# Kernel tuning notes

Measured on AMD Instinct MI355X. Metric: run time of the kernel, lower is better.

The kernel has to match this reference:

```python
import jax, jax.numpy as jnp
import numpy as np

Q_ZERO = 8  # Q4_0 zero point: w = scale * (q - 8)


def setup_inputs() -> dict:
    key = jax.random.key(0)
    k_x, k_q, k_s, k_b = jax.random.split(key, 4)
    out_f, in_f, block = 11008, 4096, 32
    n_blocks = in_f // block  # 128
    x = jax.random.normal(k_x, (1, 16, in_f), dtype=jnp.float32)
    # 4-bit quantized values per block (0..15), stored as int32 for jax friendliness
    qweight = jax.random.randint(k_q, (out_f, n_blocks, block), 0, 16, dtype=jnp.int32)
    # per-block fp scales (small, like real ggml scales)
    scales = jax.random.uniform(k_s, (out_f, n_blocks), dtype=jnp.float32) * 0.02
    bias = jax.random.normal(k_b, (out_f,), dtype=jnp.float32) * 0.01
    return {"x": x, "qweight": qweight, "scales": scales, "bias": bias}


def reference(x, qweight, scales, bias):
    # ggml_dequantize (Q4_0): w = scale * (q - 8), per block of 32 along infeatures
    out_f, n_blocks, block = qweight.shape
    w = scales[:, :, None] * (qweight.astype(jnp.float32) - Q_ZERO)  # [out, nb, 32]
    w = w.reshape(out_f, n_blocks * block)  # [out, in]
    # x @ W.T + bias, preserving leading dims
    y = jnp.einsum("bsi,oi->bso", x, w) + bias
    return y
```

## Files before the change

kernel.cpp:

```cpp
#include <hip/hip_runtime.h>
#include <stdint.h>


typedef __attribute__((ext_vector_type(8))) short bf16x8;
typedef __attribute__((ext_vector_type(4))) float f32x4;

#define OUT_F 11008
#define IN_F  4096
#define NB    128
#define KSPLIT 8
#define QB_BLK (NB / KSPLIT)
#define QB_WV  (QB_BLK / 4)
#define NTILES (OUT_F / 16)
#define M_TOK 16

__global__ __launch_bounds__(256, 4)
void qgemm_kernel(const float* __restrict__ x,
                  const int* __restrict__ qw,
                  const float* __restrict__ scales,
                  const float* __restrict__ bias,
                  float* __restrict__ out,
                  float* __restrict__ part) {
  __shared__ uint4 stage[4][QB_WV][128];
  __shared__ float red[4][256];

  const int bid  = blockIdx.x;
  const int kq   = bid & (KSPLIT - 1);
  const int ob   = (bid >> 3) << 4;
  const int tid  = threadIdx.x;
  const int wave = tid >> 6;
  const int lane = tid & 63;
  const int col  = lane & 15;
  const int kr   = lane >> 4;

  const int kb0 = kq * QB_BLK + wave * QB_WV;

  const char* qrow = (const char*)(qw + (size_t)(ob + col) * IN_F)
                   + (size_t)kb0 * 128 + kr * 32;

#pragma unroll
  for (int s = 0; s < QB_WV; ++s) {
    __builtin_amdgcn_global_load_lds(
        (const __attribute__((address_space(1))) void*)(qrow + s * 128),
        (__attribute__((address_space(3))) void*)(&stage[wave][s][0]),
        16, 0, 0);
    __builtin_amdgcn_global_load_lds(
        (const __attribute__((address_space(1))) void*)(qrow + s * 128 + 16),
        (__attribute__((address_space(3))) void*)(&stage[wave][s][64]),
        16, 0, 0);
  }

  const float* xb = x + col * IN_F + kb0 * 32 + kr * 8;
  f32x4 xv[QB_WV][2];
#pragma unroll
  for (int s = 0; s < QB_WV; ++s) {
    xv[s][0] = *(const f32x4*)(xb + s * 32);
    xv[s][1] = *(const f32x4*)(xb + s * 32 + 4);
  }
  f32x4 sv = *(const f32x4*)(scales + (ob + col) * NB + kb0);

  __syncthreads();

  f32x4 acc = {0.f, 0.f, 0.f, 0.f};
#pragma unroll
  for (int s = 0; s < QB_WV; ++s) {
    uint4 q0 = stage[wave][s][lane];
    uint4 q1 = stage[wave][s][64 + lane];
    float sc  = sv[s];
    float m8s = -8.f * sc;
    union { uint32_t u[4]; bf16x8 v; } A, B;
    uint32_t a0 = __float_as_uint(xv[s][0].x) + 0x8000u;
    uint32_t a1 = __float_as_uint(xv[s][0].y) + 0x8000u;
    uint32_t a2 = __float_as_uint(xv[s][0].z) + 0x8000u;
    uint32_t a3 = __float_as_uint(xv[s][0].w) + 0x8000u;
    uint32_t a4 = __float_as_uint(xv[s][1].x) + 0x8000u;
    uint32_t a5 = __float_as_uint(xv[s][1].y) + 0x8000u;
    uint32_t a6 = __float_as_uint(xv[s][1].z) + 0x8000u;
    uint32_t a7 = __float_as_uint(xv[s][1].w) + 0x8000u;
    A.u[0] = __builtin_amdgcn_perm(a1, a0, 0x07060302u);
    A.u[1] = __builtin_amdgcn_perm(a3, a2, 0x07060302u);
    A.u[2] = __builtin_amdgcn_perm(a5, a4, 0x07060302u);
    A.u[3] = __builtin_amdgcn_perm(a7, a6, 0x07060302u);
    uint32_t w0 = __float_as_uint(fmaf((float)(int)q0.x, sc, m8s));
    uint32_t w1 = __float_as_uint(fmaf((float)(int)q0.y, sc, m8s));
    uint32_t w2 = __float_as_uint(fmaf((float)(int)q0.z, sc, m8s));
    uint32_t w3 = __float_as_uint(fmaf((float)(int)q0.w, sc, m8s));
    uint32_t w4 = __float_as_uint(fmaf((float)(int)q1.x, sc, m8s));
    uint32_t w5 = __float_as_uint(fmaf((float)(int)q1.y, sc, m8s));
    uint32_t w6 = __float_as_uint(fmaf((float)(int)q1.z, sc, m8s));
    uint32_t w7 = __float_as_uint(fmaf((float)(int)q1.w, sc, m8s));
    B.u[0] = __builtin_amdgcn_perm(w1, w0, 0x07060302u);
    B.u[1] = __builtin_amdgcn_perm(w3, w2, 0x07060302u);
    B.u[2] = __builtin_amdgcn_perm(w5, w4, 0x07060302u);
    B.u[3] = __builtin_amdgcn_perm(w7, w6, 0x07060302u);
    acc = __builtin_amdgcn_mfma_f32_16x16x32_bf16(A.v, B.v, acc, 0, 0, 0);
  }

#pragma unroll
  for (int r = 0; r < 4; ++r)
    red[wave][(kr * 4 + r) * 16 + col] = acc[r];
  __syncthreads();

  float v = red[0][tid] + red[1][tid] + red[2][tid] + red[3][tid];
  if (part) {
    part[(size_t)bid * 256 + tid] = v;
  } else {
    int t = tid >> 4;
    int o = ob + (tid & 15);
    if (kq == 0) v += bias[o];
    __hip_atomic_fetch_add(out + (size_t)t * OUT_F + o, v, __ATOMIC_RELAXED,
                           __HIP_MEMORY_SCOPE_AGENT);
  }
}

__global__ __launch_bounds__(256)
void reduce_kernel(const float* __restrict__ part,
                   const float* __restrict__ bias,
                   float* __restrict__ out) {
  int idx = blockIdx.x * 256 + threadIdx.x;
  int t = idx / OUT_F;
  int o = idx - t * OUT_F;
  const float* p = part + (size_t)(o >> 4) * (KSPLIT * 256)
                 + ((t << 4) | (o & 15));
  float acc = bias[o];
#pragma unroll
  for (int kq = 0; kq < KSPLIT; ++kq)
    acc += p[kq * 256];
  out[idx] = acc;
}

extern "C" void kernel_launch(void* const* d_in, const int* in_sizes, int n_in,
                              void* d_out, int out_size, void* d_ws, size_t ws_size,
                              hipStream_t stream) {
  const float* x      = (const float*)d_in[0];
  const int*   qw     = (const int*)d_in[1];
  const float* scales = (const float*)d_in[2];
  const float* bias   = (const float*)d_in[3];
  float* out = (float*)d_out;

  const size_t need = (size_t)NTILES * KSPLIT * 256 * sizeof(float);
  if (d_ws != nullptr && ws_size >= need) {
    float* part = (float*)d_ws;
    qgemm_kernel<<<NTILES * KSPLIT, 256, 0, stream>>>(x, qw, scales, bias,
                                                      nullptr, part);
    reduce_kernel<<<(M_TOK * OUT_F) / 256, 256, 0, stream>>>(part, bias, out);
  } else {
    hipMemsetAsync(out, 0, (size_t)M_TOK * OUT_F * sizeof(float), stream);
    qgemm_kernel<<<NTILES * KSPLIT, 256, 0, stream>>>(x, qw, scales, bias,
                                                      out, nullptr);
  }
}
```

Measured before the change: 254.5 us.

## Double-buffer weight staging across K chunks and halve the split-K factor

Each block now walks four chunks of its K range instead of doing a single load-then-compute step. The next chunk's weights are staged into LDS with global_load_lds, and its activations and scales are prefetched into registers, while the current chunk is computed, using two LDS buffers. KSPLIT drops from 8 to 4, which halves the grid size and the partial-sum traffic that the reduce kernel reads. The risks are a barrier per chunk and fewer blocks in flight to hide memory latency.

```diff
diff --git a/kernel.cpp b/kernel.cpp
--- a/kernel.cpp
+++ b/kernel.cpp
@@ -8,10 +8,11 @@
 #define OUT_F 11008
 #define IN_F  4096
 #define NB    128
-#define KSPLIT 8
-#define QB_BLK (NB / KSPLIT)
-#define QB_WV  (QB_BLK / 4)
+#define KSPLIT 4
+#define CHUNKS 4
+#define QB_IT 8
 #define NTILES (OUT_F / 16)
+#define NBLK (NTILES * KSPLIT)
 #define M_TOK 16
 
 __global__ __launch_bounds__(256, 4)
@@ -21,79 +22,102 @@
                   const float* __restrict__ bias,
                   float* __restrict__ out,
                   float* __restrict__ part) {
-  __shared__ uint4 stage[4][QB_WV][128];
+  __shared__ uint4 stage[2][QB_IT][128];
   __shared__ float red[4][256];
 
   const int bid  = blockIdx.x;
   const int kq   = bid & (KSPLIT - 1);
-  const int ob   = (bid >> 3) << 4;
+  const int ob   = (bid >> 2) << 4;
   const int tid  = threadIdx.x;
   const int wave = tid >> 6;
   const int lane = tid & 63;
   const int col  = lane & 15;
   const int kr   = lane >> 4;
 
-  const int kb0 = kq * QB_BLK + wave * QB_WV;
+  const int kb_base = kq * (NB / KSPLIT);
 
-  const char* qrow = (const char*)(qw + (size_t)(ob + col) * IN_F)
-                   + (size_t)kb0 * 128 + kr * 32;
+  const char*  qbase = (const char*)qw + (size_t)(ob + col) * (IN_F * 4) + kr * 32;
+  const float* xbase = x + col * IN_F + kr * 8;
+  const float* sbase = scales + (ob + col) * NB;
+
+  f32x4  xv[2][2][2];
+  float2 scb[2];
+
+  auto STAGE = [&](int nb, int t) {
+#pragma unroll
+    for (int q = 0; q < 2; ++q) {
+      const int slot = wave * 2 + q;
+      const int kb   = kb_base + t * QB_IT + slot;
+      const char* src = qbase + (size_t)kb * 128;
+      __builtin_amdgcn_global_load_lds(
+          (const __attribute__((address_space(1))) void*)src,
+          (__attribute__((address_space(3))) void*)(&stage[nb][slot][0]),
+          16, 0, 0);
+      __builtin_amdgcn_global_load_lds(
+          (const __attribute__((address_space(1))) void*)(src + 16),
+          (__attribute__((address_space(3))) void*)(&stage[nb][slot][64]),
+          16, 0, 0);
+    }
+  };
+  auto PREF = [&](int p, int t) {
+    const int kb0 = kb_base + t * QB_IT + wave * 2;
+#pragma unroll
+    for (int q = 0; q < 2; ++q) {
+      const float* xp = xbase + (size_t)(kb0 + q) * 32;
+      xv[p][q][0] = *(const f32x4*)xp;
+      xv[p][q][1] = *(const f32x4*)(xp + 4);
+    }
+    scb[p] = *(const float2*)(sbase + kb0);
+  };
+
+  f32x4 acc = {0.f, 0.f, 0.f, 0.f};
+
+  STAGE(0, 0);
+  PREF(0, 0);
+  __syncthreads();
 
 #pragma unroll
-  for (int s = 0; s < QB_WV; ++s) {
-    __builtin_amdgcn_global_load_lds(
-        (const __attribute__((address_space(1))) void*)(qrow + s * 128),
-        (__attribute__((address_space(3))) void*)(&stage[wave][s][0]),
-        16, 0, 0);
-    __builtin_amdgcn_global_load_lds(
-        (const __attribute__((address_space(1))) void*)(qrow + s * 128 + 16),
-        (__attribute__((address_space(3))) void*)(&stage[wave][s][64]),
-        16, 0, 0);
-  }
-
-  const float* xb = x + col * IN_F + kb0 * 32 + kr * 8;
-  f32x4 xv[QB_WV][2];
+  for (int t = 0; t < CHUNKS; ++t) {
+    const int nb = t & 1;
+    if (t + 1 < CHUNKS) {
+      STAGE(nb ^ 1, t + 1);
+      PREF(nb ^ 1, t + 1);
+    }
 #pragma unroll
-  for (int s = 0; s < QB_WV; ++s) {
-    xv[s][0] = *(const f32x4*)(xb + s * 32);
-    xv[s][1] = *(const f32x4*)(xb + s * 32 + 4);
-  }
-  f32x4 sv = *(const f32x4*)(scales + (ob + col) * NB + kb0);
-
-  __syncthreads();
-
-  f32x4 acc = {0.f, 0.f, 0.f, 0.f};
-#pragma unroll
-  for (int s = 0; s < QB_WV; ++s) {
-    uint4 q0 = stage[wave][s][lane];
-    uint4 q1 = stage[wave][s][64 + lane];
-    float sc  = sv[s];
-    float m8s = -8.f * sc;
-    union { uint32_t u[4]; bf16x8 v; } A, B;
-    uint32_t a0 = __float_as_uint(xv[s][0].x) + 0x8000u;
-    uint32_t a1 = __float_as_uint(xv[s][0].y) + 0x8000u;
-    uint32_t a2 = __float_as_uint(xv[s][0].z) + 0x8000u;
-    uint32_t a3 = __float_as_uint(xv[s][0].w) + 0x8000u;
-    uint32_t a4 = __float_as_uint(xv[s][1].x) + 0x8000u;
-    uint32_t a5 = __float_as_uint(xv[s][1].y) + 0x8000u;
-    uint32_t a6 = __float_as_uint(xv[s][1].z) + 0x8000u;
-    uint32_t a7 = __float_as_uint(xv[s][1].w) + 0x8000u;
-    A.u[0] = __builtin_amdgcn_perm(a1, a0, 0x07060302u);
-    A.u[1] = __builtin_amdgcn_perm(a3, a2, 0x07060302u);
-    A.u[2] = __builtin_amdgcn_perm(a5, a4, 0x07060302u);
-    A.u[3] = __builtin_amdgcn_perm(a7, a6, 0x07060302u);
-    uint32_t w0 = __float_as_uint(fmaf((float)(int)q0.x, sc, m8s));
-    uint32_t w1 = __float_as_uint(fmaf((float)(int)q0.y, sc, m8s));
-    uint32_t w2 = __float_as_uint(fmaf((float)(int)q0.z, sc, m8s));
-    uint32_t w3 = __float_as_uint(fmaf((float)(int)q0.w, sc, m8s));
-    uint32_t w4 = __float_as_uint(fmaf((float)(int)q1.x, sc, m8s));
-    uint32_t w5 = __float_as_uint(fmaf((float)(int)q1.y, sc, m8s));
-    uint32_t w6 = __float_as_uint(fmaf((float)(int)q1.z, sc, m8s));
-    uint32_t w7 = __float_as_uint(fmaf((float)(int)q1.w, sc, m8s));
-    B.u[0] = __builtin_amdgcn_perm(w1, w0, 0x07060302u);
-    B.u[1] = __builtin_amdgcn_perm(w3, w2, 0x07060302u);
-    B.u[2] = __builtin_amdgcn_perm(w5, w4, 0x07060302u);
-    B.u[3] = __builtin_amdgcn_perm(w7, w6, 0x07060302u);
-    acc = __builtin_amdgcn_mfma_f32_16x16x32_bf16(A.v, B.v, acc, 0, 0, 0);
+    for (int q = 0; q < 2; ++q) {
+      const int slot = wave * 2 + q;
+      uint4 q0 = stage[nb][slot][lane];
+      uint4 q1 = stage[nb][slot][64 + lane];
+      float sc  = (q == 0) ? scb[nb].x : scb[nb].y;
+      float m8s = -8.f * sc;
+      union { uint32_t u[4]; bf16x8 v; } A, B;
+      uint32_t a0 = __float_as_uint(xv[nb][q][0].x) + 0x8000u;
+      uint32_t a1 = __float_as_uint(xv[nb][q][0].y) + 0x8000u;
+      uint32_t a2 = __float_as_uint(xv[nb][q][0].z) + 0x8000u;
+      uint32_t a3 = __float_as_uint(xv[nb][q][0].w) + 0x8000u;
+      uint32_t a4 = __float_as_uint(xv[nb][q][1].x) + 0x8000u;
+      uint32_t a5 = __float_as_uint(xv[nb][q][1].y) + 0x8000u;
+      uint32_t a6 = __float_as_uint(xv[nb][q][1].z) + 0x8000u;
+      uint32_t a7 = __float_as_uint(xv[nb][q][1].w) + 0x8000u;
+      A.u[0] = __builtin_amdgcn_perm(a1, a0, 0x07060302u);
+      A.u[1] = __builtin_amdgcn_perm(a3, a2, 0x07060302u);
+      A.u[2] = __builtin_amdgcn_perm(a5, a4, 0x07060302u);
+      A.u[3] = __builtin_amdgcn_perm(a7, a6, 0x07060302u);
+      uint32_t w0 = __float_as_uint(fmaf((float)(int)q0.x, sc, m8s));
+      uint32_t w1 = __float_as_uint(fmaf((float)(int)q0.y, sc, m8s));
+      uint32_t w2 = __float_as_uint(fmaf((float)(int)q0.z, sc, m8s));
+      uint32_t w3 = __float_as_uint(fmaf((float)(int)q0.w, sc, m8s));
+      uint32_t w4 = __float_as_uint(fmaf((float)(int)q1.x, sc, m8s));
+      uint32_t w5 = __float_as_uint(fmaf((float)(int)q1.y, sc, m8s));
+      uint32_t w6 = __float_as_uint(fmaf((float)(int)q1.z, sc, m8s));
+      uint32_t w7 = __float_as_uint(fmaf((float)(int)q1.w, sc, m8s));
+      B.u[0] = __builtin_amdgcn_perm(w1, w0, 0x07060302u);
+      B.u[1] = __builtin_amdgcn_perm(w3, w2, 0x07060302u);
+      B.u[2] = __builtin_amdgcn_perm(w5, w4, 0x07060302u);
+      B.u[3] = __builtin_amdgcn_perm(w7, w6, 0x07060302u);
+      acc = __builtin_amdgcn_mfma_f32_16x16x32_bf16(A.v, B.v, acc, 0, 0, 0);
+    }
+    __syncthreads();
   }
 
 #pragma unroll
@@ -138,15 +162,13 @@
   const float* bias   = (const float*)d_in[3];
   float* out = (float*)d_out;
 
-  const size_t need = (size_t)NTILES * KSPLIT * 256 * sizeof(float);
+  const size_t need = (size_t)NBLK * 256 * sizeof(float);
   if (d_ws != nullptr && ws_size >= need) {
-    float* part = (float*)d_ws;
-    qgemm_kernel<<<NTILES * KSPLIT, 256, 0, stream>>>(x, qw, scales, bias,
-                                                      nullptr, part);
-    reduce_kernel<<<(M_TOK * OUT_F) / 256, 256, 0, stream>>>(part, bias, out);
+    float* p = (float*)d_ws;
+    qgemm_kernel<<<NBLK, 256, 0, stream>>>(x, qw, scales, bias, nullptr, p);
+    reduce_kernel<<<(M_TOK * OUT_F) / 256, 256, 0, stream>>>(p, bias, out);
   } else {
     hipMemsetAsync(out, 0, (size_t)M_TOK * OUT_F * sizeof(float), stream);
-    qgemm_kernel<<<NTILES * KSPLIT, 256, 0, stream>>>(x, qw, scales, bias,
-                                                      out, nullptr);
+    qgemm_kernel<<<NBLK, 256, 0, stream>>>(x, qw, scales, bias, out, nullptr);
   }
 }
```

Measured after the change: 256.7 us. About the same (+0.9%).
